# Kernel tuning notes

Measured on AMD Instinct MI355X. Metric: run time of the kernel, lower is better.

The kernel has to match this reference:

```python
import jax, jax.numpy as jnp
import numpy as np

B, T, C = 2, 2048, 2048
NH, NKV = 16, 4
HD = C // NH  # 128
DFF = 4 * C


def rmsnorm(x):
    eps = jnp.finfo(x.dtype).eps
    return x * jax.lax.rsqrt(jnp.mean(jnp.square(x), axis=-1, keepdims=True) + eps)


def rotary(x, cos, sin):
    # x: [B,T,H,HD], cos/sin: [1,T,1,HD//2]
    d = x.shape[-1] // 2
    x1, x2 = x[..., :d], x[..., d:]
    return jnp.concatenate([x1 * cos + x2 * sin, -x1 * sin + x2 * cos], axis=-1)


def setup_inputs() -> dict:
    key = jax.random.key(0)
    ks = jax.random.split(key, 8)
    x = jax.random.normal(ks[0], (B, T, C), jnp.float32)
    inv_freq = 1.0 / (10000.0 ** (jnp.arange(HD // 2, dtype=jnp.float32) / (HD // 2)))
    ang = jnp.arange(T, dtype=jnp.float32)[:, None] * inv_freq[None, :]  # [T, HD//2]
    cos = jnp.cos(ang)[None, :, None, :]
    sin = jnp.sin(ang)[None, :, None, :]
    s = 0.02
    wq = jax.random.normal(ks[1], (C, NH * HD), jnp.float32) * s
    wk = jax.random.normal(ks[2], (C, NKV * HD), jnp.float32) * s
    wv = jax.random.normal(ks[3], (C, NKV * HD), jnp.float32) * s
    wo = jax.random.normal(ks[4], (C, C), jnp.float32) * s
    w_fc = jax.random.normal(ks[5], (C, DFF), jnp.float32) * s
    w_proj = jax.random.normal(ks[6], (DFF, C), jnp.float32) * s
    return {"x": x, "cos": cos, "sin": sin, "wq": wq, "wk": wk, "wv": wv,
            "wo": wo, "w_fc": w_fc, "w_proj": w_proj}


def reference(x, cos, sin, wq, wk, wv, wo, w_fc, w_proj):
    # --- attention sublayer (pre-norm residual) ---
    h = rmsnorm(x)
    q = (h @ wq).reshape(B, T, NH, HD)
    k = (h @ wk).reshape(B, T, NKV, HD)
    v = (h @ wv).reshape(B, T, NKV, HD)
    q = rmsnorm(rotary(q, cos, sin))
    k = rmsnorm(rotary(k, cos, sin))
    rep = NH // NKV
    k = jnp.repeat(k, rep, axis=2)  # [B,T,NH,HD]
    v = jnp.repeat(v, rep, axis=2)
    scale = 1.0 / np.sqrt(HD)
    scores = jnp.einsum('bqhd,bkhd->bhqk', q, k) * scale
    causal = jnp.tril(jnp.ones((T, T), dtype=bool))
    scores = jnp.where(causal[None, None], scores, jnp.finfo(scores.dtype).min)
    attn = jax.nn.softmax(scores, axis=-1)
    y = jnp.einsum('bhqk,bkhd->bqhd', attn, v).reshape(B, T, C)
    x = x + y @ wo
    # --- MLP sublayer (relu^2) ---
    h = rmsnorm(x)
    h = jnp.square(jax.nn.relu(h @ w_fc))
    x = x + h @ w_proj
    return x
```

## Files before the change

### kernel.cpp

```cpp
#include <hip/hip_runtime.h>
#include <cstdint>
#include <cstddef>


#define B_    2
#define T_    2048
#define C_    2048
#define NH_   16
#define NKV_  4
#define HD_   128
#define DFF_  8192
#define EPS_  1.1920928955078125e-07f

typedef short          bf16x8 __attribute__((ext_vector_type(8)));
typedef float          f32x4  __attribute__((ext_vector_type(4)));
typedef unsigned short u16;
typedef unsigned short u16x8  __attribute__((ext_vector_type(8)));
typedef unsigned short u16x4  __attribute__((ext_vector_type(4)));

__device__ __forceinline__ u16 f2bf(float f) {
    unsigned u = __float_as_uint(f);
    unsigned r = u + 0x7fffu + ((u >> 16) & 1u);
    return (u16)(r >> 16);
}

__device__ __forceinline__ void load_lds16(const void* g, void* l) {
    __builtin_amdgcn_global_load_lds(
        (__attribute__((address_space(1))) void*)(g),
        (__attribute__((address_space(3))) void*)(l), 16, 0, 0);
}

struct TD  { const float* src; u16* dst; int K, N, boff; };
struct TD6 { TD t[6]; };

__global__ void transpose_cast_all(TD6 d) {
    int bid = blockIdx.x;
    int di = 0;
    for (int i = 5; i > 0; --i) if (bid >= d.t[i].boff) { di = i; break; }
    const float* src = d.t[di].src;
    u16* dst = d.t[di].dst;
    int K = d.t[di].K, N = d.t[di].N;
    int lb = bid - d.t[di].boff;
    int nx = N >> 5;
    int n0 = (lb % nx) * 32;
    int k0 = (lb / nx) * 32;

    __shared__ float tile[32][33];
    int tx = threadIdx.x & 31;
    int ty = threadIdx.x >> 5;
    for (int j = 0; j < 4; ++j)
        tile[ty + j * 8][tx] = src[(size_t)(k0 + ty + j * 8) * N + n0 + tx];
    __syncthreads();
    for (int j = 0; j < 4; ++j)
        dst[(size_t)(n0 + ty + j * 8) * K + k0 + tx] = f2bf(tile[tx][ty + j * 8]);
}

__global__ void transpose_v(const u16* __restrict__ vb, u16* __restrict__ Vt) {
    int bx   = blockIdx.x;
    int dblk = bx & 1;
    int t0   = (bx >> 1) * 32;
    int kvh  = blockIdx.y, b = blockIdx.z;
    int dl   = threadIdx.x & 63;
    int tc   = threadIdx.x >> 6;
    int d    = dblk * 64 + dl;
    u16x8 v8;
    for (int j = 0; j < 8; ++j) {
        int t = t0 + tc * 8 + j;
        v8[j] = vb[((size_t)(b * T_ + t) * NKV_ + kvh) * HD_ + d];
    }
    *(u16x8*)(Vt + ((size_t)((b * NKV_ + kvh) * HD_ + d)) * T_ + t0 + tc * 8) = v8;
}

__global__ void rmsnorm_rows(const float* __restrict__ x, u16* __restrict__ out) {
    int row = blockIdx.x;
    const float4* xr = (const float4*)(x + (size_t)row * C_);
    float4 a = xr[threadIdx.x];
    float4 b = xr[threadIdx.x + 256];
    float ss = a.x * a.x + a.y * a.y + a.z * a.z + a.w * a.w
             + b.x * b.x + b.y * b.y + b.z * b.z + b.w * b.w;
    for (int m = 1; m < 64; m <<= 1) ss += __shfl_xor(ss, m, 64);
    __shared__ float part[4];
    if ((threadIdx.x & 63) == 0) part[threadIdx.x >> 6] = ss;
    __syncthreads();
    float tot = part[0] + part[1] + part[2] + part[3];
    float sc = rsqrtf(tot * (1.0f / C_) + EPS_);
    u16x4 o1, o2;
    o1[0] = f2bf(a.x * sc); o1[1] = f2bf(a.y * sc); o1[2] = f2bf(a.z * sc); o1[3] = f2bf(a.w * sc);
    o2[0] = f2bf(b.x * sc); o2[1] = f2bf(b.y * sc); o2[2] = f2bf(b.z * sc); o2[3] = f2bf(b.w * sc);
    u16x4* orow = (u16x4*)(out + (size_t)row * C_);
    orow[threadIdx.x]       = o1;
    orow[threadIdx.x + 256] = o2;
}

__global__ void rope_rms2(const float* __restrict__ Xq, const float* __restrict__ Xk,
                          const float* __restrict__ cosb, const float* __restrict__ sinb,
                          u16* __restrict__ Oq, u16* __restrict__ Ok) {
    int gw   = (int)((blockIdx.x * blockDim.x + threadIdx.x) >> 6);
    int lane = threadIdx.x & 63;
    const float* X; u16* O; int t;
    if (gw < B_ * T_ * NH_) {
        X = Xq + (size_t)gw * HD_;  O = Oq + (size_t)gw * HD_;  t = (gw / NH_) % T_;
    } else {
        int w2 = gw - B_ * T_ * NH_;
        X = Xk + (size_t)w2 * HD_;  O = Ok + (size_t)w2 * HD_;  t = (w2 / NKV_) % T_;
    }
    float x1 = X[lane];
    float x2 = X[64 + lane];
    float c  = cosb[t * 64 + lane];
    float sn = sinb[t * 64 + lane];
    float r1 = x1 * c + x2 * sn;
    float r2 = x2 * c - x1 * sn;
    float ss = r1 * r1 + r2 * r2;
    for (int m = 1; m < 64; m <<= 1) ss += __shfl_xor(ss, m, 64);
    float sc = rsqrtf(ss * (1.0f / HD_) + EPS_);
    O[lane]      = f2bf(r1 * sc);
    O[64 + lane] = f2bf(r2 * sc);
}

template <int EPI>
__launch_bounds__(256, 2)
__global__ void gemm_bt(const u16* __restrict__ A, const u16* __restrict__ Bt,
                        void* __restrict__ out, const float* __restrict__ res,
                        void* __restrict__ out2, void* __restrict__ out3,
                        int M, int N, int K) {
    __shared__ __attribute__((aligned(16))) u16 As[2][128 * 32];
    __shared__ __attribute__((aligned(16))) u16 Bs[2][128 * 32];
    int tid  = threadIdx.x;
    int lane = tid & 63;
    int wave = tid >> 6;
    int quad = lane >> 4;
    int l16  = lane & 15;
    int bn = blockIdx.x, bm = blockIdx.y;
    int wm = wave >> 1, wn = wave & 1;

    int srow = lane >> 2;
    int scol = (((lane & 3) ^ (srow & 3)) ) * 8;
    const u16* Ag = A  + (size_t)(bm * 128 + wave * 32 + srow) * K + scol;
    const u16* Bg = Bt + (size_t)(bn * 128 + wave * 32 + srow) * K + scol;

    auto stage = [&](int kk, int buf) {
        u16* Ab = &As[buf][(wave * 32) * 32];
        u16* Bb = &Bs[buf][(wave * 32) * 32];
        load_lds16(Ag + kk,                  Ab);
        load_lds16(Ag + kk + (size_t)16 * K, Ab + 16 * 32);
        load_lds16(Bg + kk,                  Bb);
        load_lds16(Bg + kk + (size_t)16 * K, Bb + 16 * 32);
    };

    f32x4 zero = {0.f, 0.f, 0.f, 0.f};
    f32x4 acc[4][4];
    for (int i = 0; i < 4; ++i)
        for (int j = 0; j < 4; ++j) acc[i][j] = zero;

    int rsw = (l16 & 3);
    stage(0, 0);
    int cur = 0;
    for (int k0 = 0; k0 < K; k0 += 32, cur ^= 1) {
        __syncthreads();
        if (k0 + 32 < K) stage(k0 + 32, cur ^ 1);
        bf16x8 af[4], bfr[4];
        int cs = (quad ^ rsw) * 8;
        for (int t = 0; t < 4; ++t) {
            af[t]  = *(const bf16x8*)&As[cur][(wm * 64 + t * 16 + l16) * 32 + cs];
            bfr[t] = *(const bf16x8*)&Bs[cur][(wn * 64 + t * 16 + l16) * 32 + cs];
        }
        for (int i = 0; i < 4; ++i)
            for (int j = 0; j < 4; ++j)
                acc[i][j] = __builtin_amdgcn_mfma_f32_16x16x32_bf16(af[i], bfr[j], acc[i][j], 0, 0, 0);
    }

    for (int i = 0; i < 4; ++i)
        for (int j = 0; j < 4; ++j)
            for (int r = 0; r < 4; ++r) {
                int rg = bm * 128 + wm * 64 + i * 16 + quad * 4 + r;
                int cg = bn * 128 + wn * 64 + j * 16 + l16;
                float v = acc[i][j][r];
                if (EPI == 0) {
                    ((float*)out)[(size_t)rg * N + cg] = v;
                } else if (EPI == 1) {
                    ((u16*)out)[(size_t)rg * N + cg] = f2bf(v);
                } else if (EPI == 2) {
                    float t = fmaxf(v, 0.f);
                    ((u16*)out)[(size_t)rg * N + cg] = f2bf(t * t);
                } else if (EPI == 3) {
                    size_t idx = (size_t)rg * N + cg;
                    ((float*)out)[idx] = res[idx] + v;
                } else {
                    if (cg < 2048)      ((float*)out)[(size_t)rg * 2048 + cg] = v;
                    else if (cg < 2560) ((float*)out2)[(size_t)rg * 512 + (cg - 2048)] = v;
                    else                ((u16*)out3)[(size_t)rg * 512 + (cg - 2560)] = f2bf(v);
                }
            }
}

__launch_bounds__(256, 2)
__global__ void flash_attn2(const u16* __restrict__ Q, const u16* __restrict__ Kb,
                            const u16* __restrict__ Vt, u16* __restrict__ Y) {
    __shared__ __attribute__((aligned(16))) u16 Qs[128 * 128];
    __shared__ __attribute__((aligned(16))) u16 Ks[64 * 128];
    __shared__ __attribute__((aligned(16))) u16 Vs[128 * 64];

    int bid = blockIdx.x;
    int half = bid >> 8, idx = bid & 255;
    int qr = idx & 15;
    int qt = half ? (15 - qr) : qr;
    int bh = (idx >> 4) | (half << 4);
    int b = bh >> 4, h = bh & 15;
    int kvh = h >> 2;
    int q0 = qt * 128;

    int tid = threadIdx.x, lane = tid & 63, wave = tid >> 6;
    int quad = lane >> 4, l16 = lane & 15;

    {
        int r = lane >> 4;
        for (int c = 0; c < 8; ++c) {
            int row = wave * 32 + c * 4 + r;
            int cc = ((lane & 15) ^ (row & 15)) * 8;
            const u16* g = Q + ((size_t)((b * T_ + q0 + row) * NH_ + h)) * HD_ + cc;
            load_lds16(g, &Qs[(wave * 32 + c * 4) * 128]);
        }
    }
    __syncthreads();

    bf16x8 qf[2][4];
    for (int qtile = 0; qtile < 2; ++qtile)
        for (int kd = 0; kd < 4; ++kd)
            qf[qtile][kd] = *(const bf16x8*)&Qs[(wave * 32 + qtile * 16 + l16) * 128
                                               + (((kd * 4 + quad) ^ l16) * 8)];
    u16* Ps = &Qs[wave * 32 * 128];

    f32x4 zero = {0.f, 0.f, 0.f, 0.f};
    f32x4 o[2][8];
    for (int qtile = 0; qtile < 2; ++qtile)
        for (int dt = 0; dt < 8; ++dt) o[qtile][dt] = zero;
    float m_i[2] = {-__builtin_inff(), -__builtin_inff()};
    float l_i[2] = {0.f, 0.f};
    const float s2s = 0.08838834764831845f * 1.4426950408889634f;

    int nkt = 2 * qt + 2;
    for (int kt = 0; kt < nkt; ++kt) {
        __syncthreads();
        {
            int r = lane >> 4;
            for (int c = 0; c < 4; ++c) {
                int row = wave * 16 + c * 4 + r;
                int cc = ((lane & 15) ^ (row & 15)) * 8;
                const u16* g = Kb + ((size_t)((b * T_ + kt * 64 + row) * NKV_ + kvh)) * HD_ + cc;
                load_lds16(g, &Ks[(wave * 16 + c * 4) * 128]);
            }
        }
        {
            int dr = lane >> 3;
            int kc = (((lane & 7) ^ dr) ) * 8;
            for (int c = 0; c < 4; ++c) {
                int drow = wave * 32 + c * 8 + dr;
                const u16* g = Vt + ((size_t)((b * NKV_ + kvh) * HD_ + drow)) * T_ + kt * 64 + kc;
                load_lds16(g, &Vs[(wave * 32 + c * 8) * 64]);
            }
        }
        __syncthreads();

        f32x4 st[2][4];
        for (int qtile = 0; qtile < 2; ++qtile)
            for (int tn = 0; tn < 4; ++tn) st[qtile][tn] = zero;
        for (int tn = 0; tn < 4; ++tn)
            for (int kd = 0; kd < 4; ++kd) {
                bf16x8 kf = *(const bf16x8*)&Ks[(tn * 16 + l16) * 128
                                                + (((kd * 4 + quad) ^ l16) * 8)];
                st[0][tn] = __builtin_amdgcn_mfma_f32_16x16x32_bf16(kf, qf[0][kd], st[0][tn], 0, 0, 0);
                st[1][tn] = __builtin_amdgcn_mfma_f32_16x16x32_bf16(kf, qf[1][kd], st[1][tn], 0, 0, 0);
            }

        for (int qtile = 0; qtile < 2; ++qtile) {
            int qmin = q0 + wave * 32 + qtile * 16;
            int qg   = qmin + l16;
            bool need_mask = (kt * 64 + 63 > qmin);
            float mx = -__builtin_inff();
            for (int tn = 0; tn < 4; ++tn)
                for (int r = 0; r < 4; ++r) {
                    float v = st[qtile][tn][r] * s2s;
                    if (need_mask) {
                        int key = kt * 64 + tn * 16 + quad * 4 + r;
                        if (key > qg) v = -__builtin_inff();
                    }
                    st[qtile][tn][r] = v;
                    mx = fmaxf(mx, v);
                }
            mx = fmaxf(mx, __shfl_xor(mx, 16, 64));
            mx = fmaxf(mx, __shfl_xor(mx, 32, 64));
            float mnew = fmaxf(m_i[qtile], mx);
            float al   = exp2f(m_i[qtile] - mnew);
            m_i[qtile] = mnew;
            float sum = 0.f;
            for (int tn = 0; tn < 4; ++tn) {
                u16x4 pk;
                for (int r = 0; r < 4; ++r) {
                    float e = exp2f(st[qtile][tn][r] - mnew);
                    sum += e;
                    pk[r] = f2bf(e);
                }
                *(u16x4*)&Ps[(qtile * 16 + l16) * 72 + tn * 16 + quad * 4] = pk;
            }
            sum += __shfl_xor(sum, 16, 64);
            sum += __shfl_xor(sum, 32, 64);
            l_i[qtile] = l_i[qtile] * al + sum;
            float aB[4];
            for (int r = 0; r < 4; ++r) aB[r] = __shfl(al, quad * 4 + r, 64);
            for (int dt = 0; dt < 8; ++dt)
                for (int r = 0; r < 4; ++r) o[qtile][dt][r] *= aB[r];
        }

        bf16x8 pf[2][2];
        for (int qtile = 0; qtile < 2; ++qtile)
            for (int ks = 0; ks < 2; ++ks)
                pf[qtile][ks] = *(const bf16x8*)&Ps[(qtile * 16 + l16) * 72 + ks * 32 + quad * 8];
        for (int ks = 0; ks < 2; ++ks)
            for (int dt = 0; dt < 8; ++dt) {
                bf16x8 vf = *(const bf16x8*)&Vs[(dt * 16 + l16) * 64
                                                + (((ks * 4 + quad) ^ (l16 & 7)) * 8)];
                o[0][dt] = __builtin_amdgcn_mfma_f32_16x16x32_bf16(pf[0][ks], vf, o[0][dt], 0, 0, 0);
                o[1][dt] = __builtin_amdgcn_mfma_f32_16x16x32_bf16(pf[1][ks], vf, o[1][dt], 0, 0, 0);
            }
    }

    for (int qtile = 0; qtile < 2; ++qtile) {
        float inv = 1.0f / l_i[qtile];
        float iB[4];
        for (int r = 0; r < 4; ++r) iB[r] = __shfl(inv, quad * 4 + r, 64);
        for (int r = 0; r < 4; ++r) {
            int qg = q0 + wave * 32 + qtile * 16 + quad * 4 + r;
            u16* yr = Y + ((size_t)((b * T_ + qg) * NH_ + h)) * HD_;
            for (int dt = 0; dt < 8; ++dt)
                yr[dt * 16 + l16] = f2bf(o[qtile][dt][r] * iB[r]);
        }
    }
}

extern "C" void kernel_launch(void* const* d_in, const int* in_sizes, int n_in,
                              void* d_out, int out_size, void* d_ws, size_t ws_size,
                              hipStream_t stream) {
    const float* x     = (const float*)d_in[0];
    const float* cosb  = (const float*)d_in[1];
    const float* sinb  = (const float*)d_in[2];
    const float* wq    = (const float*)d_in[3];
    const float* wk    = (const float*)d_in[4];
    const float* wv    = (const float*)d_in[5];
    const float* wo    = (const float*)d_in[6];
    const float* wfc   = (const float*)d_in[7];
    const float* wproj = (const float*)d_in[8];

    char* ws = (char*)d_ws;
    size_t off = 0;
    auto alloc = [&](size_t bytes) { char* p = ws + off; off += (bytes + 255) & ~(size_t)255; return p; };

    u16*   wqkvT  = (u16*)alloc((size_t)3072 * C_ * 2);
    u16*   woT    = (u16*)alloc((size_t)C_ * C_ * 2);
    u16*   wfcT   = (u16*)alloc((size_t)DFF_ * C_ * 2);
    u16*   wprojT = (u16*)alloc((size_t)C_ * DFF_ * 2);
    u16*   hbuf   = (u16*)alloc((size_t)B_ * T_ * C_ * 2);
    float* x2     = (float*)alloc((size_t)B_ * T_ * C_ * 4);
    u16*   ybuf   = (u16*)alloc((size_t)B_ * T_ * C_ * 2);
    u16*   Vtb    = (u16*)alloc((size_t)B_ * NKV_ * HD_ * T_ * 2);
    char*  scratch = alloc((size_t)B_ * T_ * DFF_ * 2);
    float* q_tmp  = (float*)scratch;
    float* k_tmp  = (float*)(scratch + (size_t)B_ * T_ * C_ * 4);
    u16*   qb     = (u16*)(scratch + (size_t)B_ * T_ * C_ * 4 + (size_t)B_ * T_ * 512 * 4);
    u16*   kb     = (u16*)((char*)qb + (size_t)B_ * T_ * C_ * 2);
    u16*   vb     = (u16*)((char*)kb + (size_t)B_ * T_ * 512 * 2);
    u16*   ffbuf  = (u16*)scratch;

    const int M = B_ * T_;
    dim3 tb(256);

    TD6 td;
    td.t[0] = { wq,    wqkvT,                       C_,   C_,   0 };
    td.t[1] = { wk,    wqkvT + (size_t)2048 * C_,   C_,   512,  4096 };
    td.t[2] = { wv,    wqkvT + (size_t)2560 * C_,   C_,   512,  5120 };
    td.t[3] = { wo,    woT,                         C_,   C_,   6144 };
    td.t[4] = { wfc,   wfcT,                        C_,   DFF_, 10240 };
    td.t[5] = { wproj, wprojT,                      DFF_, C_,   26624 };
    transpose_cast_all<<<dim3(43008), tb, 0, stream>>>(td);

    rmsnorm_rows<<<M, tb, 0, stream>>>(x, hbuf);

    gemm_bt<4><<<dim3(3072 / 128, M / 128), tb, 0, stream>>>(hbuf, wqkvT, q_tmp, nullptr, k_tmp, vb, M, 3072, C_);

    rope_rms2<<<dim3((B_ * T_ * (NH_ + NKV_)) / 4), tb, 0, stream>>>(q_tmp, k_tmp, cosb, sinb, qb, kb);
    transpose_v<<<dim3(128, NKV_, B_), tb, 0, stream>>>(vb, Vtb);

    flash_attn2<<<dim3(512), tb, 0, stream>>>(qb, kb, Vtb, ybuf);

    gemm_bt<3><<<dim3(C_ / 128, M / 128), tb, 0, stream>>>(ybuf, woT, x2, x, nullptr, nullptr, M, C_, C_);

    rmsnorm_rows<<<M, tb, 0, stream>>>(x2, hbuf);

    gemm_bt<2><<<dim3(DFF_ / 128, M / 128), tb, 0, stream>>>(hbuf, wfcT, ffbuf, nullptr, nullptr, nullptr, M, DFF_, C_);

    gemm_bt<3><<<dim3(C_ / 128, M / 128), tb, 0, stream>>>(ffbuf, wprojT, d_out, x2, nullptr, nullptr, M, C_, DFF_);
}
```

Baseline: 834.7 us.

## Split-K the output projection GEMMs and fuse residual reduction into RMSNorm

```diff
diff --git a/kernel.cpp b/kernel.cpp
--- a/kernel.cpp
+++ b/kernel.cpp
@@ -22,6 +22,9 @@
     unsigned u = __float_as_uint(f);
     unsigned r = u + 0x7fffu + ((u >> 16) & 1u);
     return (u16)(r >> 16);
+}
+__device__ __forceinline__ float bf2f(u16 u) {
+    return __uint_as_float((unsigned)u << 16);
 }
 
 __device__ __forceinline__ void load_lds16(const void* g, void* l) {
@@ -92,6 +95,57 @@
     orow[threadIdx.x + 256] = o2;
 }
 
+__global__ void reduce_rms(const float* __restrict__ x, const u16* __restrict__ p0,
+                           const u16* __restrict__ p1, float* __restrict__ x2,
+                           u16* __restrict__ hout) {
+    int row = blockIdx.x;
+    const float4* xr = (const float4*)(x + (size_t)row * C_);
+    const u16x4* a0 = (const u16x4*)(p0 + (size_t)row * C_);
+    const u16x4* a1 = (const u16x4*)(p1 + (size_t)row * C_);
+    float4 v[2];
+    float ss = 0.f;
+    for (int h = 0; h < 2; ++h) {
+        int idx = threadIdx.x + h * 256;
+        float4 xv = xr[idx];
+        u16x4 b0 = a0[idx], b1 = a1[idx];
+        v[h].x = xv.x + bf2f(b0[0]) + bf2f(b1[0]);
+        v[h].y = xv.y + bf2f(b0[1]) + bf2f(b1[1]);
+        v[h].z = xv.z + bf2f(b0[2]) + bf2f(b1[2]);
+        v[h].w = xv.w + bf2f(b0[3]) + bf2f(b1[3]);
+        ss += v[h].x * v[h].x + v[h].y * v[h].y + v[h].z * v[h].z + v[h].w * v[h].w;
+    }
+    for (int m = 1; m < 64; m <<= 1) ss += __shfl_xor(ss, m, 64);
+    __shared__ float part[4];
+    if ((threadIdx.x & 63) == 0) part[threadIdx.x >> 6] = ss;
+    __syncthreads();
+    float tot = part[0] + part[1] + part[2] + part[3];
+    float sc = rsqrtf(tot * (1.0f / C_) + EPS_);
+    float4* x2r = (float4*)(x2 + (size_t)row * C_);
+    u16x4* hr   = (u16x4*)(hout + (size_t)row * C_);
+    for (int h = 0; h < 2; ++h) {
+        int idx = threadIdx.x + h * 256;
+        x2r[idx] = v[h];
+        u16x4 o;
+        o[0] = f2bf(v[h].x * sc); o[1] = f2bf(v[h].y * sc);
+        o[2] = f2bf(v[h].z * sc); o[3] = f2bf(v[h].w * sc);
+        hr[idx] = o;
+    }
+}
+
+__global__ void reduce_out(const float* __restrict__ x2, const u16* __restrict__ p0,
+                           const u16* __restrict__ p1, float* __restrict__ out) {
+    size_t i = (size_t)blockIdx.x * 256 + threadIdx.x;
+    float4 xv = ((const float4*)x2)[i];
+    u16x4 b0 = ((const u16x4*)p0)[i];
+    u16x4 b1 = ((const u16x4*)p1)[i];
+    float4 o;
+    o.x = xv.x + bf2f(b0[0]) + bf2f(b1[0]);
+    o.y = xv.y + bf2f(b0[1]) + bf2f(b1[1]);
+    o.z = xv.z + bf2f(b0[2]) + bf2f(b1[2]);
+    o.w = xv.w + bf2f(b0[3]) + bf2f(b1[3]);
+    ((float4*)out)[i] = o;
+}
+
 __global__ void rope_rms2(const float* __restrict__ Xq, const float* __restrict__ Xk,
                           const float* __restrict__ cosb, const float* __restrict__ sinb,
                           u16* __restrict__ Oq, u16* __restrict__ Ok) {
@@ -122,7 +176,7 @@
 __global__ void gemm_bt(const u16* __restrict__ A, const u16* __restrict__ Bt,
                         void* __restrict__ out, const float* __restrict__ res,
                         void* __restrict__ out2, void* __restrict__ out3,
-                        int M, int N, int K) {
+                        int M, int N, int K, int Ks) {
     __shared__ __attribute__((aligned(16))) u16 As[2][128 * 32];
     __shared__ __attribute__((aligned(16))) u16 Bs[2][128 * 32];
     int tid  = threadIdx.x;
@@ -134,17 +188,18 @@
     int wm = wave >> 1, wn = wave & 1;
 
     int srow = lane >> 2;
-    int scol = (((lane & 3) ^ (srow & 3)) ) * 8;
-    const u16* Ag = A  + (size_t)(bm * 128 + wave * 32 + srow) * K + scol;
-    const u16* Bg = Bt + (size_t)(bn * 128 + wave * 32 + srow) * K + scol;
+    int scol = (((lane & 3) ^ (srow & 3))) * 8;
+    size_t koff = (size_t)blockIdx.z * K;
+    const u16* Ag = A  + (size_t)(bm * 128 + wave * 32 + srow) * Ks + scol + koff;
+    const u16* Bg = Bt + (size_t)(bn * 128 + wave * 32 + srow) * Ks + scol + koff;
 
     auto stage = [&](int kk, int buf) {
         u16* Ab = &As[buf][(wave * 32) * 32];
         u16* Bb = &Bs[buf][(wave * 32) * 32];
-        load_lds16(Ag + kk,                  Ab);
-        load_lds16(Ag + kk + (size_t)16 * K, Ab + 16 * 32);
-        load_lds16(Bg + kk,                  Bb);
-        load_lds16(Bg + kk + (size_t)16 * K, Bb + 16 * 32);
+        load_lds16(Ag + kk,                   Ab);
+        load_lds16(Ag + kk + (size_t)16 * Ks, Ab + 16 * 32);
+        load_lds16(Bg + kk,                   Bb);
+        load_lds16(Bg + kk + (size_t)16 * Ks, Bb + 16 * 32);
     };
 
     f32x4 zero = {0.f, 0.f, 0.f, 0.f};
@@ -175,20 +230,16 @@
                 int rg = bm * 128 + wm * 64 + i * 16 + quad * 4 + r;
                 int cg = bn * 128 + wn * 64 + j * 16 + l16;
                 float v = acc[i][j][r];
-                if (EPI == 0) {
-                    ((float*)out)[(size_t)rg * N + cg] = v;
-                } else if (EPI == 1) {
-                    ((u16*)out)[(size_t)rg * N + cg] = f2bf(v);
-                } else if (EPI == 2) {
+                if (EPI == 2) {
                     float t = fmaxf(v, 0.f);
                     ((u16*)out)[(size_t)rg * N + cg] = f2bf(t * t);
-                } else if (EPI == 3) {
-                    size_t idx = (size_t)rg * N + cg;
-                    ((float*)out)[idx] = res[idx] + v;
-                } else {
+                } else if (EPI == 4) {
                     if (cg < 2048)      ((float*)out)[(size_t)rg * 2048 + cg] = v;
                     else if (cg < 2560) ((float*)out2)[(size_t)rg * 512 + (cg - 2048)] = v;
                     else                ((u16*)out3)[(size_t)rg * 512 + (cg - 2560)] = f2bf(v);
+                } else {
+                    u16* p = (blockIdx.z == 0) ? (u16*)out : (u16*)out2;
+                    p[(size_t)rg * N + cg] = f2bf(v);
                 }
             }
 }
@@ -252,7 +303,7 @@
         }
         {
             int dr = lane >> 3;
-            int kc = (((lane & 7) ^ dr) ) * 8;
+            int kc = (((lane & 7) ^ dr)) * 8;
             for (int c = 0; c < 4; ++c) {
                 int drow = wave * 32 + c * 8 + dr;
                 const u16* g = Vt + ((size_t)((b * NKV_ + kvh) * HD_ + drow)) * T_ + kt * 64 + kc;
@@ -368,6 +419,7 @@
     u16*   qb     = (u16*)(scratch + (size_t)B_ * T_ * C_ * 4 + (size_t)B_ * T_ * 512 * 4);
     u16*   kb     = (u16*)((char*)qb + (size_t)B_ * T_ * C_ * 2);
     u16*   vb     = (u16*)((char*)kb + (size_t)B_ * T_ * 512 * 2);
+    u16*   wop1   = (u16*)scratch;
     u16*   ffbuf  = (u16*)scratch;
 
     const int M = B_ * T_;
@@ -384,18 +436,20 @@
 
     rmsnorm_rows<<<M, tb, 0, stream>>>(x, hbuf);
 
-    gemm_bt<4><<<dim3(3072 / 128, M / 128), tb, 0, stream>>>(hbuf, wqkvT, q_tmp, nullptr, k_tmp, vb, M, 3072, C_);
+    gemm_bt<4><<<dim3(3072 / 128, M / 128), tb, 0, stream>>>(hbuf, wqkvT, q_tmp, nullptr, k_tmp, vb, M, 3072, C_, C_);
 
     rope_rms2<<<dim3((B_ * T_ * (NH_ + NKV_)) / 4), tb, 0, stream>>>(q_tmp, k_tmp, cosb, sinb, qb, kb);
     transpose_v<<<dim3(128, NKV_, B_), tb, 0, stream>>>(vb, Vtb);
 
     flash_attn2<<<dim3(512), tb, 0, stream>>>(qb, kb, Vtb, ybuf);
 
-    gemm_bt<3><<<dim3(C_ / 128, M / 128), tb, 0, stream>>>(ybuf, woT, x2, x, nullptr, nullptr, M, C_, C_);
-
-    rmsnorm_rows<<<M, tb, 0, stream>>>(x2, hbuf);
-
-    gemm_bt<2><<<dim3(DFF_ / 128, M / 128), tb, 0, stream>>>(hbuf, wfcT, ffbuf, nullptr, nullptr, nullptr, M, DFF_, C_);
-
-    gemm_bt<3><<<dim3(C_ / 128, M / 128), tb, 0, stream>>>(ffbuf, wprojT, d_out, x2, nullptr, nullptr, M, C_, DFF_);
-}
+    gemm_bt<5><<<dim3(C_ / 128, M / 128, 2), tb, 0, stream>>>(ybuf, woT, hbuf, nullptr, wop1, nullptr, M, C_, C_ / 2, C_);
+
+    reduce_rms<<<M, tb, 0, stream>>>(x, hbuf, wop1, x2, hbuf);
+
+    gemm_bt<2><<<dim3(DFF_ / 128, M / 128), tb, 0, stream>>>(hbuf, wfcT, ffbuf, nullptr, nullptr, nullptr, M, DFF_, C_, C_);
+
+    gemm_bt<5><<<dim3(C_ / 128, M / 128, 2), tb, 0, stream>>>(ffbuf, wprojT, hbuf, nullptr, ybuf, nullptr, M, C_, DFF_ / 2, DFF_);
+
+    reduce_out<<<dim3((M * C_) / 1024), tb, 0, stream>>>(x2, hbuf, ybuf, (float*)d_out);
+}
```

New measurement: 786.2 us. 5.8% less time.
